# Kernel tuning notes

Hardware: AMD Instinct MI355X
Metric: run time of the kernel (lower is better)

The kernel has to match this reference:

```python
import jax, jax.numpy as jnp
import numpy as np

N = 50000        # number of nodes
K = 32           # sampled neighbors per node (fixed degree)
D = 128          # input_dim
DOUT = 128       # output_dim


def setup_inputs() -> dict:
    key = jax.random.key(0)
    k1, k2, k3, k4, k5 = jax.random.split(key, 5)
    node_fea1 = jax.random.normal(k1, (N, D), dtype=jnp.float32)
    node_fea2 = jax.random.normal(k2, (N, D), dtype=jnp.float32)
    neigh_idx1 = jax.random.randint(k3, (N, K), 0, N, dtype=jnp.int32)
    neigh_idx2 = jax.random.randint(k4, (N, K), 0, N, dtype=jnp.int32)
    # xavier-uniform init for weight [4*D, DOUT]
    limit = float(np.sqrt(6.0 / (4 * D + DOUT)))
    weight = jax.random.uniform(k5, (4 * D, DOUT), dtype=jnp.float32,
                                minval=-limit, maxval=limit)
    return {"node_fea1": node_fea1, "node_fea2": node_fea2,
            "neigh_idx1": neigh_idx1, "neigh_idx2": neigh_idx2,
            "weight": weight}


def reference(node_fea1, node_fea2, neigh_idx1, neigh_idx2, weight):
    # neighbor mean aggregation of node_fea1 over the two neighbor lists
    # (forward_den reads node_fea1 in BOTH aggregation blocks)
    nei1 = node_fea1[neigh_idx1].mean(axis=1)   # [N, D]
    nei2 = node_fea1[neigh_idx2].mean(axis=1)   # [N, D]
    cat_fea = jnp.concatenate([node_fea1, node_fea2, nei1, nei2], axis=1)  # [N, 4D]
    return jnp.tanh(cat_fea @ weight)           # [N, DOUT]
```

## Files before the change

### kernel.cpp

```cpp
#include <hip/hip_runtime.h>
#include <math.h>

#define N_NODES 50000
#define KNEI    32
#define DIM     128
#define DOUT    128
#define NUNITS  (2 * N_NODES)

typedef __attribute__((ext_vector_type(8))) short short8;
typedef __attribute__((ext_vector_type(4))) float floatx4;

static __device__ __forceinline__ unsigned short f2bf(float f) {
    unsigned int u = __float_as_uint(f);
    unsigned int lsb = (u >> 16) & 1u;
    u += 0x7fffu + lsb;
    return (unsigned short)(u >> 16);
}
static __device__ __forceinline__ unsigned int pack2(float a, float b) {
    return (unsigned int)f2bf(a) | ((unsigned int)f2bf(b) << 16);
}
static __device__ __forceinline__ float fast_tanh(float x) {
    float ax = fabsf(x);
    float e  = __expf(2.0f * ax);
    float t  = 1.0f - 2.0f / (e + 1.0f);
    return copysignf(t, x);
}
static __device__ __forceinline__ unsigned int pk4_u8(float a, float b, float c,
                                                      float d, float inv) {
    int qa = ((int)rintf(a * inv) + 128) & 0xff;
    int qb = ((int)rintf(b * inv) + 128) & 0xff;
    int qc = ((int)rintf(c * inv) + 128) & 0xff;
    int qd = ((int)rintf(d * inv) + 128) & 0xff;
    return (unsigned int)(qa | (qb << 8) | (qc << 16) | (qd << 24));
}


__global__ __launch_bounds__(256) void convert_i8(
    const float* __restrict__ src, unsigned int* __restrict__ Q8,
    float* __restrict__ Sc)
{
    int t = blockIdx.x * 256 + threadIdx.x;
    if (t >= N_NODES * 8) return;
    int node = t >> 3, j = t & 7;
    const float* rp = src + node * DIM + j * 16;
    float4 v0 = *(const float4*)rp;
    float4 v1 = *(const float4*)(rp + 4);
    float4 v2 = *(const float4*)(rp + 8);
    float4 v3 = *(const float4*)(rp + 12);

    float am = fabsf(v0.x);
    am = fmaxf(am, fabsf(v0.y)); am = fmaxf(am, fabsf(v0.z)); am = fmaxf(am, fabsf(v0.w));
    am = fmaxf(am, fabsf(v1.x)); am = fmaxf(am, fabsf(v1.y));
    am = fmaxf(am, fabsf(v1.z)); am = fmaxf(am, fabsf(v1.w));
    am = fmaxf(am, fabsf(v2.x)); am = fmaxf(am, fabsf(v2.y));
    am = fmaxf(am, fabsf(v2.z)); am = fmaxf(am, fabsf(v2.w));
    am = fmaxf(am, fabsf(v3.x)); am = fmaxf(am, fabsf(v3.y));
    am = fmaxf(am, fabsf(v3.z)); am = fmaxf(am, fabsf(v3.w));
    #pragma unroll
    for (int d = 1; d < 8; d <<= 1) am = fmaxf(am, __shfl_xor(am, d, 64));

    float inv = (am > 1e-30f) ? 127.0f / am : 0.0f;
    int4 o;
    o.x = (int)pk4_u8(v0.x, v0.y, v0.z, v0.w, inv);
    o.y = (int)pk4_u8(v1.x, v1.y, v1.z, v1.w, inv);
    o.z = (int)pk4_u8(v2.x, v2.y, v2.z, v2.w, inv);
    o.w = (int)pk4_u8(v3.x, v3.y, v3.z, v3.w, inv);
    *(int4*)(Q8 + node * 32 + j * 4) = o;
    if (j == 0) Sc[node] = am * (1.0f / 127.0f);
}

__global__ __launch_bounds__(256) void transpose_w(
    const float* __restrict__ W, unsigned short* __restrict__ Wt)
{
    int t = blockIdx.x * 256 + threadIdx.x;
    int k = t >> 7, n = t & 127;
    Wt[n * 512 + k] = f2bf(W[t]);
}

__global__ __launch_bounds__(256) void aggregate_i8(
    const unsigned char* __restrict__ Q8,
    const float* __restrict__ Sc,
    const int* __restrict__ idx1,
    const int* __restrict__ idx2,
    unsigned short* __restrict__ NEI)
{
    __shared__ int   idxs[32][40];
    __shared__ float scs[32][40];

    const int tid = threadIdx.x;
    const int bu0 = blockIdx.x * 32;
    const int ul  = tid >> 3;
    const int l   = tid & 7;

    {
        int uu = bu0 + ul;
        const int* ip = ((uu & 1) ? idx2 : idx1) + (uu >> 1) * KNEI + l * 4;
        int4 v = *(const int4*)ip;
        *(int4*)&idxs[ul][l * 4] = v;
    }
    __syncthreads();

    {
        #pragma unroll
        for (int k = 0; k < 4; ++k)
            scs[ul][l * 4 + k] = Sc[idxs[ul][l * 4 + k]];
    }
    __syncthreads();

    const int u    = bu0 + ul;
    const int node = u >> 1;
    const int list = u & 1;

    const unsigned char* base = Q8 + l * 16;
    float sums[16];
    #pragma unroll
    for (int i = 0; i < 16; ++i) sums[i] = 0.f;
    float ssum = 0.f;

    #pragma unroll 2
    for (int b = 0; b < 4; ++b) {
        int4 i4a = *(const int4*)&idxs[ul][b * 8];
        int4 i4b = *(const int4*)&idxs[ul][b * 8 + 4];
        int rows[8] = {i4a.x, i4a.y, i4a.z, i4a.w,
                       i4b.x, i4b.y, i4b.z, i4b.w};
        int4 v[8];
        #pragma unroll
        for (int j = 0; j < 8; ++j)
            v[j] = *(const int4*)(base + (size_t)rows[j] * 128);

        float4 sA = *(const float4*)&scs[ul][b * 8];
        float4 sB = *(const float4*)&scs[ul][b * 8 + 4];
        float sc8[8] = {sA.x, sA.y, sA.z, sA.w, sB.x, sB.y, sB.z, sB.w};
        ssum += sA.x + sA.y + sA.z + sA.w + sB.x + sB.y + sB.z + sB.w;

        #pragma unroll
        for (int j = 0; j < 8; ++j) {
            float s = sc8[j];
            unsigned int d[4] = {(unsigned int)v[j].x, (unsigned int)v[j].y,
                                 (unsigned int)v[j].z, (unsigned int)v[j].w};
            #pragma unroll
            for (int jj = 0; jj < 4; ++jj) {
                unsigned int w = d[jj];
                sums[4 * jj + 0] = fmaf(s, (float)(w & 0xffu),         sums[4 * jj + 0]);
                sums[4 * jj + 1] = fmaf(s, (float)((w >> 8) & 0xffu),  sums[4 * jj + 1]);
                sums[4 * jj + 2] = fmaf(s, (float)((w >> 16) & 0xffu), sums[4 * jj + 2]);
                sums[4 * jj + 3] = fmaf(s, (float)(w >> 24),           sums[4 * jj + 3]);
            }
        }
    }

    const float invK = 1.0f / 32.0f;
    const float corr = 128.0f * ssum;
    #pragma unroll
    for (int i = 0; i < 16; ++i) sums[i] = (sums[i] - corr) * invK;

    int4 o0, o1;
    o0.x = (int)pack2(sums[0],  sums[1]);
    o0.y = (int)pack2(sums[2],  sums[3]);
    o0.z = (int)pack2(sums[4],  sums[5]);
    o0.w = (int)pack2(sums[6],  sums[7]);
    o1.x = (int)pack2(sums[8],  sums[9]);
    o1.y = (int)pack2(sums[10], sums[11]);
    o1.z = (int)pack2(sums[12], sums[13]);
    o1.w = (int)pack2(sums[14], sums[15]);
    unsigned short* op = NEI + node * 256 + list * 128 + l * 16;
    *(int4*)op       = o0;
    *(int4*)(op + 8) = o1;
}

__global__ __launch_bounds__(256) void gemm128(
    const float*          __restrict__ fea1,
    const float*          __restrict__ fea2,
    const unsigned short* __restrict__ NEI,
    const unsigned short* __restrict__ Wt,
    float* __restrict__ out)
{
    __shared__ unsigned short As[128][72];
    __shared__ unsigned short Bs[128][72];

    const int tid  = threadIdx.x;
    const int w    = tid >> 6;
    const int lane = tid & 63;
    const int m0   = blockIdx.x * 128;
    const int wm   = (w & 1) * 64;
    const int wn   = (w >> 1) * 64;
    const int lm   = lane & 15;
    const int lk   = (lane >> 4) * 8;

    floatx4 acc[4][4];
    #pragma unroll
    for (int i = 0; i < 4; ++i)
        #pragma unroll
        for (int j = 0; j < 4; ++j)
            acc[i][j] = (floatx4){0.f, 0.f, 0.f, 0.f};

    for (int cc = 0; cc < 8; ++cc) {
        const int kb = cc * 64;
        if (cc < 4) {
            const float* src = (cc < 2) ? fea1 : fea2;
            const int cbase = (cc & 1) * 64;
            #pragma unroll
            for (int i = 0; i < 8; ++i) {
                int f   = tid + i * 256;
                int row = f >> 4;
                int c4  = (f & 15) * 4;
                int node = m0 + row;
                if (node >= N_NODES) node = N_NODES - 1;
                float4 v = *(const float4*)(src + node * DIM + cbase + c4);
                *(unsigned int*)&As[row][c4 + 0] = pack2(v.x, v.y);
                *(unsigned int*)&As[row][c4 + 2] = pack2(v.z, v.w);
            }
        } else {
            const int cb = kb - 256;
            #pragma unroll
            for (int i = 0; i < 4; ++i) {
                int sl  = tid + i * 256;
                int row = sl >> 3;
                int o8  = (sl & 7) * 8;
                int node = m0 + row;
                if (node >= N_NODES) node = N_NODES - 1;
                *(int4*)&As[row][o8] = *(const int4*)(NEI + node * 256 + cb + o8);
            }
        }
        #pragma unroll
        for (int i = 0; i < 4; ++i) {
            int sl  = tid + i * 256;
            int row = sl >> 3;
            int o8  = (sl & 7) * 8;
            *(int4*)&Bs[row][o8] = *(const int4*)(Wt + row * 512 + kb + o8);
        }
        __syncthreads();

        #pragma unroll
        for (int ks = 0; ks < 64; ks += 32) {
            short8 af[4], bf_[4];
            #pragma unroll
            for (int im = 0; im < 4; ++im)
                af[im] = *(const short8*)&As[wm + im * 16 + lm][ks + lk];
            #pragma unroll
            for (int in = 0; in < 4; ++in)
                bf_[in] = *(const short8*)&Bs[wn + in * 16 + lm][ks + lk];
            #pragma unroll
            for (int im = 0; im < 4; ++im)
                #pragma unroll
                for (int in = 0; in < 4; ++in)
                    acc[im][in] = __builtin_amdgcn_mfma_f32_16x16x32_bf16(
                        af[im], bf_[in], acc[im][in], 0, 0, 0);
        }
        __syncthreads();
    }

    #pragma unroll
    for (int im = 0; im < 4; ++im) {
        int rbase = m0 + wm + im * 16 + (lane >> 4) * 4;
        #pragma unroll
        for (int in = 0; in < 4; ++in) {
            int col = wn + in * 16 + lm;
            #pragma unroll
            for (int r = 0; r < 4; ++r) {
                int node = rbase + r;
                if (node < N_NODES)
                    out[node * DOUT + col] = fast_tanh(acc[im][in][r]);
            }
        }
    }
}

#define MT      64
#define KC      64
#define AS_STRIDE 68

__global__ __launch_bounds__(256) void sage_fused_fb(
    const float* __restrict__ fea1, const float* __restrict__ fea2,
    const int* __restrict__ idx1, const int* __restrict__ idx2,
    const float* __restrict__ W, float* __restrict__ out)
{
    __shared__ float As[KC][AS_STRIDE];
    __shared__ int   idxs[MT][64];
    const int tid = threadIdx.x;
    const int n0  = blockIdx.x * MT;
    #pragma unroll
    for (int i = 0; i < 8; ++i) {
        int e = tid + i * 256, m = e >> 5, kk = e & 31;
        int node = n0 + m; if (node >= N_NODES) node = N_NODES - 1;
        idxs[m][kk]      = idx1[node * KNEI + kk];
        idxs[m][32 + kk] = idx2[node * KNEI + kk];
    }
    float acc[8][4];
    #pragma unroll
    for (int i = 0; i < 8; ++i)
        #pragma unroll
        for (int j = 0; j < 4; ++j) acc[i][j] = 0.f;
    const int j0 = (tid & 31) * 4;
    const int m0 = (tid >> 5) * 8;
    for (int c = 0; c < 8; ++c) {
        if (c < 4) {
            const float* src = (c < 2) ? fea1 : fea2;
            const int cbase = (c & 1) * 64;
            #pragma unroll
            for (int i = 0; i < 4; ++i) {
                int f = tid + i * 256, m = f >> 4, c4 = (f & 15) * 4;
                int node = n0 + m; if (node >= N_NODES) node = N_NODES - 1;
                float4 v = *(const float4*)(src + node * DIM + cbase + c4);
                As[c4 + 0][m] = v.x; As[c4 + 1][m] = v.y;
                As[c4 + 2][m] = v.z; As[c4 + 3][m] = v.w;
            }
        } else {
            const int col = tid & 63, kbase = (c & 1) * 64;
            const int lbase = (c < 6) ? 0 : 32, g = tid >> 6;
            for (int mm = 0; mm < 16; ++mm) {
                const int m = g * 16 + mm;
                const int4* ip = (const int4*)&idxs[m][lbase];
                float s = 0.f;
                #pragma unroll
                for (int q = 0; q < 8; ++q) {
                    int4 nb = ip[q];
                    s += fea1[nb.x * DIM + kbase + col];
                    s += fea1[nb.y * DIM + kbase + col];
                    s += fea1[nb.z * DIM + kbase + col];
                    s += fea1[nb.w * DIM + kbase + col];
                }
                As[col][m] = s * (1.0f / 32.0f);
            }
        }
        __syncthreads();
        const float* wp = W + (c * KC) * DOUT + j0;
        #pragma unroll 4
        for (int k = 0; k < KC; ++k) {
            float4 w4 = *(const float4*)(wp + k * DOUT);
            const float4* ap = (const float4*)&As[k][m0];
            float4 a0 = ap[0]; float4 a1 = ap[1];
            float av[8] = {a0.x, a0.y, a0.z, a0.w, a1.x, a1.y, a1.z, a1.w};
            #pragma unroll
            for (int i = 0; i < 8; ++i) {
                acc[i][0] += av[i] * w4.x; acc[i][1] += av[i] * w4.y;
                acc[i][2] += av[i] * w4.z; acc[i][3] += av[i] * w4.w;
            }
        }
        __syncthreads();
    }
    #pragma unroll
    for (int i = 0; i < 8; ++i) {
        int node = n0 + m0 + i;
        if (node < N_NODES) {
            float4 r;
            r.x = tanhf(acc[i][0]); r.y = tanhf(acc[i][1]);
            r.z = tanhf(acc[i][2]); r.w = tanhf(acc[i][3]);
            *(float4*)(out + node * DOUT + j0) = r;
        }
    }
}

extern "C" void kernel_launch(void* const* d_in, const int* in_sizes, int n_in,
                              void* d_out, int out_size, void* d_ws, size_t ws_size,
                              hipStream_t stream) {
    const float* fea1 = (const float*)d_in[0];
    const float* fea2 = (const float*)d_in[1];
    const int*   idx1 = (const int*)d_in[2];
    const int*   idx2 = (const int*)d_in[3];
    const float* W    = (const float*)d_in[4];
    float* out = (float*)d_out;

    const size_t Q8_BYTES  = (size_t)N_NODES * DIM;
    const size_t SC_BYTES  = (size_t)N_NODES * 4;
    const size_t NEI_BYTES = (size_t)N_NODES * 256 * 2;
    const size_t WT_BYTES  = (size_t)512 * 128 * 2;

    if (ws_size >= Q8_BYTES + SC_BYTES + NEI_BYTES + WT_BYTES) {
        unsigned char*  Q8  = (unsigned char*)d_ws;
        float*          Scp = (float*)((char*)d_ws + Q8_BYTES);
        unsigned short* NEI = (unsigned short*)((char*)d_ws + Q8_BYTES + SC_BYTES);
        unsigned short* Wt  = (unsigned short*)((char*)d_ws + Q8_BYTES + SC_BYTES + NEI_BYTES);

        convert_i8<<<(N_NODES * 8 + 255) / 256, 256, 0, stream>>>(
            fea1, (unsigned int*)Q8, Scp);
        transpose_w<<<512 * 128 / 256, 256, 0, stream>>>(W, Wt);
        aggregate_i8<<<NUNITS / 32, 256, 0, stream>>>(Q8, Scp, idx1, idx2, NEI);
        gemm128<<<(N_NODES + 127) / 128, 256, 0, stream>>>(fea1, fea2, NEI, Wt, out);
    } else {
        const int grid = (N_NODES + MT - 1) / MT;
        sage_fused_fb<<<grid, 256, 0, stream>>>(fea1, fea2, idx1, idx2, W, out);
    }
}
```

Baseline: 165.4 us.

## Fuse neighbor aggregation into GEMM and merge conversion kernels

The int8 neighbor gather-mean now runs inside the GEMM's K-loop and writes straight into the shared A tile, so the bf16 NEI intermediate is never written to or read back from global memory. The GEMM M-tile shrinks from 128 to 64 rows to raise the block count. The feature quantization and weight transpose are merged into one launch, cutting the pipeline from four kernels to two. In exchange, each block's aggregation phase is serialized with its MFMA phase, with no separate high-occupancy gather kernel to hide gather latency, and the scale loads are now per-thread global reads.

```diff
diff --git a/kernel.cpp b/kernel.cpp
--- a/kernel.cpp
+++ b/kernel.cpp
@@ -5,7 +5,6 @@
 #define KNEI    32
 #define DIM     128
 #define DOUT    128
-#define NUNITS  (2 * N_NODES)
 
 typedef __attribute__((ext_vector_type(8))) short short8;
 typedef __attribute__((ext_vector_type(4))) float floatx4;
@@ -35,14 +34,22 @@
 }
 
 
-__global__ __launch_bounds__(256) void convert_i8(
-    const float* __restrict__ src, unsigned int* __restrict__ Q8,
-    float* __restrict__ Sc)
+__global__ __launch_bounds__(256) void convert_both(
+    const float* __restrict__ fea1, const float* __restrict__ W,
+    unsigned int* __restrict__ Q8, float* __restrict__ Sc,
+    unsigned short* __restrict__ Wt)
 {
-    int t = blockIdx.x * 256 + threadIdx.x;
+    int b = blockIdx.x;
+    if (b >= 1563) {
+        int t = (b - 1563) * 256 + threadIdx.x;
+        int k = t >> 7, n = t & 127;
+        Wt[n * 512 + k] = f2bf(W[t]);
+        return;
+    }
+    int t = b * 256 + threadIdx.x;
     if (t >= N_NODES * 8) return;
     int node = t >> 3, j = t & 7;
-    const float* rp = src + node * DIM + j * 16;
+    const float* rp = fea1 + node * DIM + j * 16;
     float4 v0 = *(const float4*)rp;
     float4 v1 = *(const float4*)(rp + 4);
     float4 v2 = *(const float4*)(rp + 8);
@@ -69,138 +76,49 @@
     if (j == 0) Sc[node] = am * (1.0f / 127.0f);
 }
 
-__global__ __launch_bounds__(256) void transpose_w(
-    const float* __restrict__ W, unsigned short* __restrict__ Wt)
-{
-    int t = blockIdx.x * 256 + threadIdx.x;
-    int k = t >> 7, n = t & 127;
-    Wt[n * 512 + k] = f2bf(W[t]);
-}
-
-__global__ __launch_bounds__(256) void aggregate_i8(
-    const unsigned char* __restrict__ Q8,
-    const float* __restrict__ Sc,
-    const int* __restrict__ idx1,
-    const int* __restrict__ idx2,
-    unsigned short* __restrict__ NEI)
-{
-    __shared__ int   idxs[32][40];
-    __shared__ float scs[32][40];
-
-    const int tid = threadIdx.x;
-    const int bu0 = blockIdx.x * 32;
-    const int ul  = tid >> 3;
-    const int l   = tid & 7;
-
-    {
-        int uu = bu0 + ul;
-        const int* ip = ((uu & 1) ? idx2 : idx1) + (uu >> 1) * KNEI + l * 4;
-        int4 v = *(const int4*)ip;
-        *(int4*)&idxs[ul][l * 4] = v;
-    }
-    __syncthreads();
-
-    {
-        #pragma unroll
-        for (int k = 0; k < 4; ++k)
-            scs[ul][l * 4 + k] = Sc[idxs[ul][l * 4 + k]];
-    }
-    __syncthreads();
-
-    const int u    = bu0 + ul;
-    const int node = u >> 1;
-    const int list = u & 1;
-
-    const unsigned char* base = Q8 + l * 16;
-    float sums[16];
-    #pragma unroll
-    for (int i = 0; i < 16; ++i) sums[i] = 0.f;
-    float ssum = 0.f;
-
-    #pragma unroll 2
-    for (int b = 0; b < 4; ++b) {
-        int4 i4a = *(const int4*)&idxs[ul][b * 8];
-        int4 i4b = *(const int4*)&idxs[ul][b * 8 + 4];
-        int rows[8] = {i4a.x, i4a.y, i4a.z, i4a.w,
-                       i4b.x, i4b.y, i4b.z, i4b.w};
-        int4 v[8];
-        #pragma unroll
-        for (int j = 0; j < 8; ++j)
-            v[j] = *(const int4*)(base + (size_t)rows[j] * 128);
-
-        float4 sA = *(const float4*)&scs[ul][b * 8];
-        float4 sB = *(const float4*)&scs[ul][b * 8 + 4];
-        float sc8[8] = {sA.x, sA.y, sA.z, sA.w, sB.x, sB.y, sB.z, sB.w};
-        ssum += sA.x + sA.y + sA.z + sA.w + sB.x + sB.y + sB.z + sB.w;
-
-        #pragma unroll
-        for (int j = 0; j < 8; ++j) {
-            float s = sc8[j];
-            unsigned int d[4] = {(unsigned int)v[j].x, (unsigned int)v[j].y,
-                                 (unsigned int)v[j].z, (unsigned int)v[j].w};
-            #pragma unroll
-            for (int jj = 0; jj < 4; ++jj) {
-                unsigned int w = d[jj];
-                sums[4 * jj + 0] = fmaf(s, (float)(w & 0xffu),         sums[4 * jj + 0]);
-                sums[4 * jj + 1] = fmaf(s, (float)((w >> 8) & 0xffu),  sums[4 * jj + 1]);
-                sums[4 * jj + 2] = fmaf(s, (float)((w >> 16) & 0xffu), sums[4 * jj + 2]);
-                sums[4 * jj + 3] = fmaf(s, (float)(w >> 24),           sums[4 * jj + 3]);
-            }
-        }
-    }
-
-    const float invK = 1.0f / 32.0f;
-    const float corr = 128.0f * ssum;
-    #pragma unroll
-    for (int i = 0; i < 16; ++i) sums[i] = (sums[i] - corr) * invK;
-
-    int4 o0, o1;
-    o0.x = (int)pack2(sums[0],  sums[1]);
-    o0.y = (int)pack2(sums[2],  sums[3]);
-    o0.z = (int)pack2(sums[4],  sums[5]);
-    o0.w = (int)pack2(sums[6],  sums[7]);
-    o1.x = (int)pack2(sums[8],  sums[9]);
-    o1.y = (int)pack2(sums[10], sums[11]);
-    o1.z = (int)pack2(sums[12], sums[13]);
-    o1.w = (int)pack2(sums[14], sums[15]);
-    unsigned short* op = NEI + node * 256 + list * 128 + l * 16;
-    *(int4*)op       = o0;
-    *(int4*)(op + 8) = o1;
-}
-
-__global__ __launch_bounds__(256) void gemm128(
+__global__ __launch_bounds__(256) void gemm_fused(
     const float*          __restrict__ fea1,
     const float*          __restrict__ fea2,
-    const unsigned short* __restrict__ NEI,
+    const unsigned char*  __restrict__ Q8,
+    const float*          __restrict__ Sc,
+    const int*            __restrict__ idx1,
+    const int*            __restrict__ idx2,
     const unsigned short* __restrict__ Wt,
     float* __restrict__ out)
 {
-    __shared__ unsigned short As[128][72];
+    __shared__ unsigned short As[64][72];
     __shared__ unsigned short Bs[128][72];
 
     const int tid  = threadIdx.x;
     const int w    = tid >> 6;
     const int lane = tid & 63;
-    const int m0   = blockIdx.x * 128;
-    const int wm   = (w & 1) * 64;
+    const int m0   = blockIdx.x * 64;
+    const int wm   = (w & 1) * 32;
     const int wn   = (w >> 1) * 64;
     const int lm   = lane & 15;
     const int lk   = (lane >> 4) * 8;
 
-    floatx4 acc[4][4];
-    #pragma unroll
-    for (int i = 0; i < 4; ++i)
+    floatx4 acc[2][4];
+    #pragma unroll
+    for (int i = 0; i < 2; ++i)
         #pragma unroll
         for (int j = 0; j < 4; ++j)
             acc[i][j] = (floatx4){0.f, 0.f, 0.f, 0.f};
 
     for (int cc = 0; cc < 8; ++cc) {
         const int kb = cc * 64;
+        #pragma unroll
+        for (int i = 0; i < 4; ++i) {
+            int sl  = tid + i * 256;
+            int row = sl >> 3;
+            int o8  = (sl & 7) * 8;
+            *(int4*)&Bs[row][o8] = *(const int4*)(Wt + row * 512 + kb + o8);
+        }
         if (cc < 4) {
             const float* src = (cc < 2) ? fea1 : fea2;
             const int cbase = (cc & 1) * 64;
             #pragma unroll
-            for (int i = 0; i < 8; ++i) {
+            for (int i = 0; i < 4; ++i) {
                 int f   = tid + i * 256;
                 int row = f >> 4;
                 int c4  = (f & 15) * 4;
@@ -211,37 +129,82 @@
                 *(unsigned int*)&As[row][c4 + 2] = pack2(v.z, v.w);
             }
         } else {
-            const int cb = kb - 256;
-            #pragma unroll
-            for (int i = 0; i < 4; ++i) {
-                int sl  = tid + i * 256;
-                int row = sl >> 3;
-                int o8  = (sl & 7) * 8;
-                int node = m0 + row;
-                if (node >= N_NODES) node = N_NODES - 1;
-                *(int4*)&As[row][o8] = *(const int4*)(NEI + node * 256 + cb + o8);
-            }
-        }
-        #pragma unroll
-        for (int i = 0; i < 4; ++i) {
-            int sl  = tid + i * 256;
-            int row = sl >> 3;
-            int o8  = (sl & 7) * 8;
-            *(int4*)&Bs[row][o8] = *(const int4*)(Wt + row * 512 + kb + o8);
+            const int* ibase = (cc >= 6) ? idx2 : idx1;
+            const int cb = (cc & 1) * 64;
+            const int g  = tid >> 2;
+            const int l2 = tid & 3;
+            int node = m0 + g;
+            if (node >= N_NODES) node = N_NODES - 1;
+            const int4* ip = (const int4*)(ibase + node * KNEI);
+            int4 I[8];
+            #pragma unroll
+            for (int q = 0; q < 8; ++q) I[q] = ip[q];
+
+            const unsigned char* qb = Q8 + cb + l2 * 16;
+            float sums[16];
+            #pragma unroll
+            for (int i = 0; i < 16; ++i) sums[i] = 0.f;
+            float ssum = 0.f;
+
+            #pragma unroll 2
+            for (int q = 0; q < 8; ++q) {
+                int r4[4] = {I[q].x, I[q].y, I[q].z, I[q].w};
+                #pragma unroll
+                for (int t4 = 0; t4 < 4; ++t4) {
+                    unsigned int row = (unsigned int)r4[t4];
+                    uint4 v = *(const uint4*)(qb + row * 128u);
+                    float s = Sc[row];
+                    ssum += s;
+                    unsigned int d0 = v.x, d1 = v.y, d2 = v.z, d3 = v.w;
+                    sums[0]  = fmaf(s, (float)(d0 & 0xffu),         sums[0]);
+                    sums[1]  = fmaf(s, (float)((d0 >> 8) & 0xffu),  sums[1]);
+                    sums[2]  = fmaf(s, (float)((d0 >> 16) & 0xffu), sums[2]);
+                    sums[3]  = fmaf(s, (float)(d0 >> 24),           sums[3]);
+                    sums[4]  = fmaf(s, (float)(d1 & 0xffu),         sums[4]);
+                    sums[5]  = fmaf(s, (float)((d1 >> 8) & 0xffu),  sums[5]);
+                    sums[6]  = fmaf(s, (float)((d1 >> 16) & 0xffu), sums[6]);
+                    sums[7]  = fmaf(s, (float)(d1 >> 24),           sums[7]);
+                    sums[8]  = fmaf(s, (float)(d2 & 0xffu),         sums[8]);
+                    sums[9]  = fmaf(s, (float)((d2 >> 8) & 0xffu),  sums[9]);
+                    sums[10] = fmaf(s, (float)((d2 >> 16) & 0xffu), sums[10]);
+                    sums[11] = fmaf(s, (float)(d2 >> 24),           sums[11]);
+                    sums[12] = fmaf(s, (float)(d3 & 0xffu),         sums[12]);
+                    sums[13] = fmaf(s, (float)((d3 >> 8) & 0xffu),  sums[13]);
+                    sums[14] = fmaf(s, (float)((d3 >> 16) & 0xffu), sums[14]);
+                    sums[15] = fmaf(s, (float)(d3 >> 24),           sums[15]);
+                }
+            }
+            const float inv32 = 1.0f / 32.0f;
+            const float corr  = 128.0f * ssum;
+            #pragma unroll
+            for (int i = 0; i < 16; ++i) sums[i] = (sums[i] - corr) * inv32;
+
+            unsigned short* ap = &As[g][l2 * 16];
+            int4 oA, oB;
+            oA.x = (int)pack2(sums[0],  sums[1]);
+            oA.y = (int)pack2(sums[2],  sums[3]);
+            oA.z = (int)pack2(sums[4],  sums[5]);
+            oA.w = (int)pack2(sums[6],  sums[7]);
+            oB.x = (int)pack2(sums[8],  sums[9]);
+            oB.y = (int)pack2(sums[10], sums[11]);
+            oB.z = (int)pack2(sums[12], sums[13]);
+            oB.w = (int)pack2(sums[14], sums[15]);
+            *(int4*)ap       = oA;
+            *(int4*)(ap + 8) = oB;
         }
         __syncthreads();
 
         #pragma unroll
         for (int ks = 0; ks < 64; ks += 32) {
-            short8 af[4], bf_[4];
-            #pragma unroll
-            for (int im = 0; im < 4; ++im)
+            short8 af[2], bf_[4];
+            #pragma unroll
+            for (int im = 0; im < 2; ++im)
                 af[im] = *(const short8*)&As[wm + im * 16 + lm][ks + lk];
             #pragma unroll
             for (int in = 0; in < 4; ++in)
                 bf_[in] = *(const short8*)&Bs[wn + in * 16 + lm][ks + lk];
             #pragma unroll
-            for (int im = 0; im < 4; ++im)
+            for (int im = 0; im < 2; ++im)
                 #pragma unroll
                 for (int in = 0; in < 4; ++in)
                     acc[im][in] = __builtin_amdgcn_mfma_f32_16x16x32_bf16(
@@ -251,7 +214,7 @@
     }
 
     #pragma unroll
-    for (int im = 0; im < 4; ++im) {
+    for (int im = 0; im < 2; ++im) {
         int rbase = m0 + wm + im * 16 + (lane >> 4) * 4;
         #pragma unroll
         for (int in = 0; in < 4; ++in) {
@@ -363,20 +326,17 @@
 
     const size_t Q8_BYTES  = (size_t)N_NODES * DIM;
     const size_t SC_BYTES  = (size_t)N_NODES * 4;
-    const size_t NEI_BYTES = (size_t)N_NODES * 256 * 2;
     const size_t WT_BYTES  = (size_t)512 * 128 * 2;
 
-    if (ws_size >= Q8_BYTES + SC_BYTES + NEI_BYTES + WT_BYTES) {
+    if (ws_size >= Q8_BYTES + SC_BYTES + WT_BYTES) {
         unsigned char*  Q8  = (unsigned char*)d_ws;
         float*          Scp = (float*)((char*)d_ws + Q8_BYTES);
-        unsigned short* NEI = (unsigned short*)((char*)d_ws + Q8_BYTES + SC_BYTES);
-        unsigned short* Wt  = (unsigned short*)((char*)d_ws + Q8_BYTES + SC_BYTES + NEI_BYTES);
-
-        convert_i8<<<(N_NODES * 8 + 255) / 256, 256, 0, stream>>>(
-            fea1, (unsigned int*)Q8, Scp);
-        transpose_w<<<512 * 128 / 256, 256, 0, stream>>>(W, Wt);
-        aggregate_i8<<<NUNITS / 32, 256, 0, stream>>>(Q8, Scp, idx1, idx2, NEI);
-        gemm128<<<(N_NODES + 127) / 128, 256, 0, stream>>>(fea1, fea2, NEI, Wt, out);
+        unsigned short* Wt  = (unsigned short*)((char*)d_ws + Q8_BYTES + SC_BYTES);
+
+        convert_both<<<1563 + 256, 256, 0, stream>>>(
+            fea1, W, (unsigned int*)Q8, Scp, Wt);
+        gemm_fused<<<(N_NODES + 63) / 64, 256, 0, stream>>>(
+            fea1, fea2, Q8, Scp, idx1, idx2, Wt, out);
     } else {
         const int grid = (N_NODES + MT - 1) / MT;
         sage_fused_fb<<<grid, 256, 0, stream>>>(fea1, fea2, idx1, idx2, W, out);
```

Result: slower. 239.2 us (+44.6%).

## Split int8 feature table into two column planes and aggregate per plane

Applied to the files above, without the earlier changes.

The quantized int8 feature table is stored as two 64-byte column planes, and the neighbor aggregation runs as two launches, each gathering one plane. Each launch's gather working set is then 3.2 MB instead of 6.4 MB, which is meant to improve cache hit rates for the random row gathers. The quantize kernel and the weight transpose are merged into one launch, and the index loads and output stores now use nontemporal hints. The cost is an extra launch, a second read of the index lists and scales, and 64-byte gathers that may use memory transactions less efficiently.

```diff
diff --git a/kernel.cpp b/kernel.cpp
--- a/kernel.cpp
+++ b/kernel.cpp
@@ -9,6 +9,7 @@
 
 typedef __attribute__((ext_vector_type(8))) short short8;
 typedef __attribute__((ext_vector_type(4))) float floatx4;
+typedef __attribute__((ext_vector_type(4))) int  intx4;
 
 static __device__ __forceinline__ unsigned short f2bf(float f) {
     unsigned int u = __float_as_uint(f);
@@ -35,14 +36,22 @@
 }
 
 
-__global__ __launch_bounds__(256) void convert_i8(
-    const float* __restrict__ src, unsigned int* __restrict__ Q8,
-    float* __restrict__ Sc)
+__global__ __launch_bounds__(256) void convert_both(
+    const float* __restrict__ fea1, const float* __restrict__ W,
+    unsigned char* __restrict__ Q8, float* __restrict__ Sc,
+    unsigned short* __restrict__ Wt)
 {
-    int t = blockIdx.x * 256 + threadIdx.x;
+    int b = blockIdx.x;
+    if (b >= 1563) {
+        int t = (b - 1563) * 256 + threadIdx.x;
+        int k = t >> 7, n = t & 127;
+        Wt[n * 512 + k] = f2bf(W[t]);
+        return;
+    }
+    int t = b * 256 + threadIdx.x;
     if (t >= N_NODES * 8) return;
     int node = t >> 3, j = t & 7;
-    const float* rp = src + node * DIM + j * 16;
+    const float* rp = fea1 + node * DIM + j * 16;
     float4 v0 = *(const float4*)rp;
     float4 v1 = *(const float4*)(rp + 4);
     float4 v2 = *(const float4*)(rp + 8);
@@ -60,58 +69,63 @@
     for (int d = 1; d < 8; d <<= 1) am = fmaxf(am, __shfl_xor(am, d, 64));
 
     float inv = (am > 1e-30f) ? 127.0f / am : 0.0f;
-    int4 o;
-    o.x = (int)pk4_u8(v0.x, v0.y, v0.z, v0.w, inv);
-    o.y = (int)pk4_u8(v1.x, v1.y, v1.z, v1.w, inv);
-    o.z = (int)pk4_u8(v2.x, v2.y, v2.z, v2.w, inv);
-    o.w = (int)pk4_u8(v3.x, v3.y, v3.z, v3.w, inv);
-    *(int4*)(Q8 + node * 32 + j * 4) = o;
+    uint4 o;
+    o.x = pk4_u8(v0.x, v0.y, v0.z, v0.w, inv);
+    o.y = pk4_u8(v1.x, v1.y, v1.z, v1.w, inv);
+    o.z = pk4_u8(v2.x, v2.y, v2.z, v2.w, inv);
+    o.w = pk4_u8(v3.x, v3.y, v3.z, v3.w, inv);
+    unsigned char* qp = Q8 + (size_t)(j >> 2) * (N_NODES * 64)
+                           + (size_t)node * 64 + (j & 3) * 16;
+    *(uint4*)qp = o;
     if (j == 0) Sc[node] = am * (1.0f / 127.0f);
 }
 
-__global__ __launch_bounds__(256) void transpose_w(
-    const float* __restrict__ W, unsigned short* __restrict__ Wt)
-{
-    int t = blockIdx.x * 256 + threadIdx.x;
-    int k = t >> 7, n = t & 127;
-    Wt[n * 512 + k] = f2bf(W[t]);
-}
-
-__global__ __launch_bounds__(256) void aggregate_i8(
+__global__ __launch_bounds__(256) void aggregate_plane(
     const unsigned char* __restrict__ Q8,
     const float* __restrict__ Sc,
     const int* __restrict__ idx1,
     const int* __restrict__ idx2,
-    unsigned short* __restrict__ NEI)
+    unsigned short* __restrict__ NEI,
+    const int plane)
 {
-    __shared__ int   idxs[32][40];
-    __shared__ float scs[32][40];
+    __shared__ int   idxs[64][36];
+    __shared__ float scs[64][36];
 
     const int tid = threadIdx.x;
-    const int bu0 = blockIdx.x * 32;
-    const int ul  = tid >> 3;
-    const int l   = tid & 7;
-
-    {
-        int uu = bu0 + ul;
-        const int* ip = ((uu & 1) ? idx2 : idx1) + (uu >> 1) * KNEI + l * 4;
-        int4 v = *(const int4*)ip;
-        *(int4*)&idxs[ul][l * 4] = v;
+    const int bu0 = blockIdx.x * 64;
+    const int ul  = tid >> 2;
+    const int l   = tid & 3;
+
+    #pragma unroll
+    for (int i = 0; i < 2; ++i) {
+        int s   = tid + i * 256;
+        int us  = s >> 3;
+        int off = (s & 7) * 4;
+        int uu  = bu0 + us;
+        if (uu >= NUNITS) uu = NUNITS - 1;
+        const int* ip = ((uu & 1) ? idx2 : idx1) + (uu >> 1) * KNEI + off;
+        intx4 v = __builtin_nontemporal_load((const intx4*)ip);
+        *(intx4*)&idxs[us][off] = v;
     }
     __syncthreads();
 
-    {
+    #pragma unroll
+    for (int i = 0; i < 2; ++i) {
+        int s   = tid + i * 256;
+        int us  = s >> 3;
+        int off = (s & 7) * 4;
         #pragma unroll
         for (int k = 0; k < 4; ++k)
-            scs[ul][l * 4 + k] = Sc[idxs[ul][l * 4 + k]];
+            scs[us][off + k] = Sc[idxs[us][off + k]];
     }
     __syncthreads();
 
     const int u    = bu0 + ul;
-    const int node = u >> 1;
-    const int list = u & 1;
-
-    const unsigned char* base = Q8 + l * 16;
+    const int cu   = (u < NUNITS) ? u : (NUNITS - 1);
+    const int node = cu >> 1;
+    const int list = cu & 1;
+
+    const unsigned char* qb = Q8 + (size_t)plane * (N_NODES * 64) + l * 16;
     float sums[16];
     #pragma unroll
     for (int i = 0; i < 16; ++i) sums[i] = 0.f;
@@ -123,10 +137,10 @@
         int4 i4b = *(const int4*)&idxs[ul][b * 8 + 4];
         int rows[8] = {i4a.x, i4a.y, i4a.z, i4a.w,
                        i4b.x, i4b.y, i4b.z, i4b.w};
-        int4 v[8];
+        uint4 v[8];
         #pragma unroll
         for (int j = 0; j < 8; ++j)
-            v[j] = *(const int4*)(base + (size_t)rows[j] * 128);
+            v[j] = *(const uint4*)(qb + (size_t)rows[j] * 64);
 
         float4 sA = *(const float4*)&scs[ul][b * 8];
         float4 sB = *(const float4*)&scs[ul][b * 8 + 4];
@@ -136,16 +150,23 @@
         #pragma unroll
         for (int j = 0; j < 8; ++j) {
             float s = sc8[j];
-            unsigned int d[4] = {(unsigned int)v[j].x, (unsigned int)v[j].y,
-                                 (unsigned int)v[j].z, (unsigned int)v[j].w};
-            #pragma unroll
-            for (int jj = 0; jj < 4; ++jj) {
-                unsigned int w = d[jj];
-                sums[4 * jj + 0] = fmaf(s, (float)(w & 0xffu),         sums[4 * jj + 0]);
-                sums[4 * jj + 1] = fmaf(s, (float)((w >> 8) & 0xffu),  sums[4 * jj + 1]);
-                sums[4 * jj + 2] = fmaf(s, (float)((w >> 16) & 0xffu), sums[4 * jj + 2]);
-                sums[4 * jj + 3] = fmaf(s, (float)(w >> 24),           sums[4 * jj + 3]);
-            }
+            unsigned int d0 = v[j].x, d1 = v[j].y, d2 = v[j].z, d3 = v[j].w;
+            sums[0]  = fmaf(s, (float)(d0 & 0xffu),         sums[0]);
+            sums[1]  = fmaf(s, (float)((d0 >> 8) & 0xffu),  sums[1]);
+            sums[2]  = fmaf(s, (float)((d0 >> 16) & 0xffu), sums[2]);
+            sums[3]  = fmaf(s, (float)(d0 >> 24),           sums[3]);
+            sums[4]  = fmaf(s, (float)(d1 & 0xffu),         sums[4]);
+            sums[5]  = fmaf(s, (float)((d1 >> 8) & 0xffu),  sums[5]);
+            sums[6]  = fmaf(s, (float)((d1 >> 16) & 0xffu), sums[6]);
+            sums[7]  = fmaf(s, (float)(d1 >> 24),           sums[7]);
+            sums[8]  = fmaf(s, (float)(d2 & 0xffu),         sums[8]);
+            sums[9]  = fmaf(s, (float)((d2 >> 8) & 0xffu),  sums[9]);
+            sums[10] = fmaf(s, (float)((d2 >> 16) & 0xffu), sums[10]);
+            sums[11] = fmaf(s, (float)(d2 >> 24),           sums[11]);
+            sums[12] = fmaf(s, (float)(d3 & 0xffu),         sums[12]);
+            sums[13] = fmaf(s, (float)((d3 >> 8) & 0xffu),  sums[13]);
+            sums[14] = fmaf(s, (float)((d3 >> 16) & 0xffu), sums[14]);
+            sums[15] = fmaf(s, (float)(d3 >> 24),           sums[15]);
         }
     }
 
@@ -154,18 +175,20 @@
     #pragma unroll
     for (int i = 0; i < 16; ++i) sums[i] = (sums[i] - corr) * invK;
 
-    int4 o0, o1;
-    o0.x = (int)pack2(sums[0],  sums[1]);
-    o0.y = (int)pack2(sums[2],  sums[3]);
-    o0.z = (int)pack2(sums[4],  sums[5]);
-    o0.w = (int)pack2(sums[6],  sums[7]);
-    o1.x = (int)pack2(sums[8],  sums[9]);
-    o1.y = (int)pack2(sums[10], sums[11]);
-    o1.z = (int)pack2(sums[12], sums[13]);
-    o1.w = (int)pack2(sums[14], sums[15]);
-    unsigned short* op = NEI + node * 256 + list * 128 + l * 16;
-    *(int4*)op       = o0;
-    *(int4*)(op + 8) = o1;
+    if (u < NUNITS) {
+        intx4 o0, o1;
+        o0.x = (int)pack2(sums[0],  sums[1]);
+        o0.y = (int)pack2(sums[2],  sums[3]);
+        o0.z = (int)pack2(sums[4],  sums[5]);
+        o0.w = (int)pack2(sums[6],  sums[7]);
+        o1.x = (int)pack2(sums[8],  sums[9]);
+        o1.y = (int)pack2(sums[10], sums[11]);
+        o1.z = (int)pack2(sums[12], sums[13]);
+        o1.w = (int)pack2(sums[14], sums[15]);
+        unsigned short* op = NEI + node * 256 + list * 128 + plane * 64 + l * 16;
+        __builtin_nontemporal_store(o0, (intx4*)op);
+        __builtin_nontemporal_store(o1, (intx4*)(op + 8));
+    }
 }
 
 __global__ __launch_bounds__(256) void gemm128(
@@ -372,10 +395,10 @@
         unsigned short* NEI = (unsigned short*)((char*)d_ws + Q8_BYTES + SC_BYTES);
         unsigned short* Wt  = (unsigned short*)((char*)d_ws + Q8_BYTES + SC_BYTES + NEI_BYTES);
 
-        convert_i8<<<(N_NODES * 8 + 255) / 256, 256, 0, stream>>>(
-            fea1, (unsigned int*)Q8, Scp);
-        transpose_w<<<512 * 128 / 256, 256, 0, stream>>>(W, Wt);
-        aggregate_i8<<<NUNITS / 32, 256, 0, stream>>>(Q8, Scp, idx1, idx2, NEI);
+        convert_both<<<1563 + 256, 256, 0, stream>>>(fea1, W, Q8, Scp, Wt);
+        const int agrid = (NUNITS + 63) / 64;
+        aggregate_plane<<<agrid, 256, 0, stream>>>(Q8, Scp, idx1, idx2, NEI, 0);
+        aggregate_plane<<<agrid, 256, 0, stream>>>(Q8, Scp, idx1, idx2, NEI, 1);
         gemm128<<<(N_NODES + 127) / 128, 256, 0, stream>>>(fea1, fea2, NEI, Wt, out);
     } else {
         const int grid = (N_NODES + MT - 1) / MT;
```

Result: slower. 193.0 us (+16.7%).

## Split GEMM and co-schedule self-feature half with neighbor aggregation

Applied to the files above, without the earlier changes.

Merges the int8 conversion and weight transpose into one launch. Splits the GEMM so the fea1/fea2 half of K runs in the same launch as the gather aggregation, writing fp32 partial sums to a workspace. A second GEMM handles the neighbor half and adds the partials before tanh. The aim is to overlap compute-bound MFMA blocks with the memory-latency-bound gather and to cut launch count. In exchange it writes and reads back a 25.6 MB fp32 partial buffer, and the larger shared-memory footprint may lower aggregation occupancy.

```diff
diff --git a/kernel.cpp b/kernel.cpp
--- a/kernel.cpp
+++ b/kernel.cpp
@@ -6,6 +6,9 @@
 #define DIM     128
 #define DOUT    128
 #define NUNITS  (2 * N_NODES)
+
+#define GP1_BLOCKS 391
+#define AGG_BLOCKS (NUNITS / 32)
 
 typedef __attribute__((ext_vector_type(8))) short short8;
 typedef __attribute__((ext_vector_type(4))) float floatx4;
@@ -35,14 +38,22 @@
 }
 
 
-__global__ __launch_bounds__(256) void convert_i8(
-    const float* __restrict__ src, unsigned int* __restrict__ Q8,
-    float* __restrict__ Sc)
+__global__ __launch_bounds__(256) void convert_both(
+    const float* __restrict__ fea1, const float* __restrict__ W,
+    unsigned int* __restrict__ Q8, float* __restrict__ Sc,
+    unsigned short* __restrict__ Wt)
 {
-    int t = blockIdx.x * 256 + threadIdx.x;
+    int b = blockIdx.x;
+    if (b >= 1563) {
+        int t = (b - 1563) * 256 + threadIdx.x;
+        int k = t >> 7, n = t & 127;
+        Wt[n * 512 + k] = f2bf(W[t]);
+        return;
+    }
+    int t = b * 256 + threadIdx.x;
     if (t >= N_NODES * 8) return;
     int node = t >> 3, j = t & 7;
-    const float* rp = src + node * DIM + j * 16;
+    const float* rp = fea1 + node * DIM + j * 16;
     float4 v0 = *(const float4*)rp;
     float4 v1 = *(const float4*)(rp + 4);
     float4 v2 = *(const float4*)(rp + 8);
@@ -69,26 +80,103 @@
     if (j == 0) Sc[node] = am * (1.0f / 127.0f);
 }
 
-__global__ __launch_bounds__(256) void transpose_w(
-    const float* __restrict__ W, unsigned short* __restrict__ Wt)
+__global__ __launch_bounds__(256) void agg_or_gemmp1(
+    const float*          __restrict__ fea1,
+    const float*          __restrict__ fea2,
+    const unsigned char*  __restrict__ Q8,
+    const float*          __restrict__ Sc,
+    const int*            __restrict__ idx1,
+    const int*            __restrict__ idx2,
+    const unsigned short* __restrict__ Wt,
+    unsigned short*       __restrict__ NEI,
+    float*                __restrict__ part)
 {
-    int t = blockIdx.x * 256 + threadIdx.x;
-    int k = t >> 7, n = t & 127;
-    Wt[n * 512 + k] = f2bf(W[t]);
-}
-
-__global__ __launch_bounds__(256) void aggregate_i8(
-    const unsigned char* __restrict__ Q8,
-    const float* __restrict__ Sc,
-    const int* __restrict__ idx1,
-    const int* __restrict__ idx2,
-    unsigned short* __restrict__ NEI)
-{
-    __shared__ int   idxs[32][40];
-    __shared__ float scs[32][40];
-
+    __shared__ unsigned char smem[36864];
     const int tid = threadIdx.x;
-    const int bu0 = blockIdx.x * 32;
+
+    if (blockIdx.x < GP1_BLOCKS) {
+        unsigned short (*As)[72] = (unsigned short(*)[72])smem;
+        unsigned short (*Bs)[72] = (unsigned short(*)[72])(smem + 18432);
+
+        const int w    = tid >> 6;
+        const int lane = tid & 63;
+        const int m0   = blockIdx.x * 128;
+        const int wm   = (w & 1) * 64;
+        const int wn   = (w >> 1) * 64;
+        const int lm   = lane & 15;
+        const int lk   = (lane >> 4) * 8;
+
+        floatx4 acc[4][4];
+        #pragma unroll
+        for (int i = 0; i < 4; ++i)
+            #pragma unroll
+            for (int j = 0; j < 4; ++j)
+                acc[i][j] = (floatx4){0.f, 0.f, 0.f, 0.f};
+
+        for (int cc = 0; cc < 4; ++cc) {
+            const int kb = cc * 64;
+            const float* src = (cc < 2) ? fea1 : fea2;
+            const int cbase = (cc & 1) * 64;
+            #pragma unroll
+            for (int i = 0; i < 8; ++i) {
+                int f   = tid + i * 256;
+                int row = f >> 4;
+                int c4  = (f & 15) * 4;
+                int node = m0 + row;
+                if (node >= N_NODES) node = N_NODES - 1;
+                float4 v = *(const float4*)(src + node * DIM + cbase + c4);
+                *(unsigned int*)&As[row][c4 + 0] = pack2(v.x, v.y);
+                *(unsigned int*)&As[row][c4 + 2] = pack2(v.z, v.w);
+            }
+            #pragma unroll
+            for (int i = 0; i < 4; ++i) {
+                int sl  = tid + i * 256;
+                int row = sl >> 3;
+                int o8  = (sl & 7) * 8;
+                *(int4*)&Bs[row][o8] = *(const int4*)(Wt + row * 512 + kb + o8);
+            }
+            __syncthreads();
+
+            #pragma unroll
+            for (int ks = 0; ks < 64; ks += 32) {
+                short8 af[4], bf_[4];
+                #pragma unroll
+                for (int im = 0; im < 4; ++im)
+                    af[im] = *(const short8*)&As[wm + im * 16 + lm][ks + lk];
+                #pragma unroll
+                for (int in = 0; in < 4; ++in)
+                    bf_[in] = *(const short8*)&Bs[wn + in * 16 + lm][ks + lk];
+                #pragma unroll
+                for (int im = 0; im < 4; ++im)
+                    #pragma unroll
+                    for (int in = 0; in < 4; ++in)
+                        acc[im][in] = __builtin_amdgcn_mfma_f32_16x16x32_bf16(
+                            af[im], bf_[in], acc[im][in], 0, 0, 0);
+            }
+            __syncthreads();
+        }
+
+        #pragma unroll
+        for (int im = 0; im < 4; ++im) {
+            int rbase = m0 + wm + im * 16 + (lane >> 4) * 4;
+            #pragma unroll
+            for (int in = 0; in < 4; ++in) {
+                int col = wn + in * 16 + lm;
+                #pragma unroll
+                for (int r = 0; r < 4; ++r) {
+                    int node = rbase + r;
+                    if (node < N_NODES)
+                        part[node * DOUT + col] = acc[im][in][r];
+                }
+            }
+        }
+        return;
+    }
+
+    int (*idxs)[40]  = (int(*)[40])smem;
+    float (*scs)[40] = (float(*)[40])(smem + 5120);
+
+    const int bu0 = (blockIdx.x - GP1_BLOCKS) * 32;
     const int ul  = tid >> 3;
     const int l   = tid & 7;
 
@@ -99,7 +187,6 @@
         *(int4*)&idxs[ul][l * 4] = v;
     }
     __syncthreads();
-
     {
         #pragma unroll
         for (int k = 0; k < 4; ++k)
@@ -123,10 +210,10 @@
         int4 i4b = *(const int4*)&idxs[ul][b * 8 + 4];
         int rows[8] = {i4a.x, i4a.y, i4a.z, i4a.w,
                        i4b.x, i4b.y, i4b.z, i4b.w};
-        int4 v[8];
+        uint4 v[8];
         #pragma unroll
         for (int j = 0; j < 8; ++j)
-            v[j] = *(const int4*)(base + (size_t)rows[j] * 128);
+            v[j] = *(const uint4*)(base + (size_t)rows[j] * 128);
 
         float4 sA = *(const float4*)&scs[ul][b * 8];
         float4 sB = *(const float4*)&scs[ul][b * 8 + 4];
@@ -136,16 +223,23 @@
         #pragma unroll
         for (int j = 0; j < 8; ++j) {
             float s = sc8[j];
-            unsigned int d[4] = {(unsigned int)v[j].x, (unsigned int)v[j].y,
-                                 (unsigned int)v[j].z, (unsigned int)v[j].w};
-            #pragma unroll
-            for (int jj = 0; jj < 4; ++jj) {
-                unsigned int w = d[jj];
-                sums[4 * jj + 0] = fmaf(s, (float)(w & 0xffu),         sums[4 * jj + 0]);
-                sums[4 * jj + 1] = fmaf(s, (float)((w >> 8) & 0xffu),  sums[4 * jj + 1]);
-                sums[4 * jj + 2] = fmaf(s, (float)((w >> 16) & 0xffu), sums[4 * jj + 2]);
-                sums[4 * jj + 3] = fmaf(s, (float)(w >> 24),           sums[4 * jj + 3]);
-            }
+            unsigned int d0 = v[j].x, d1 = v[j].y, d2 = v[j].z, d3 = v[j].w;
+            sums[0]  = fmaf(s, (float)(d0 & 0xffu),         sums[0]);
+            sums[1]  = fmaf(s, (float)((d0 >> 8) & 0xffu),  sums[1]);
+            sums[2]  = fmaf(s, (float)((d0 >> 16) & 0xffu), sums[2]);
+            sums[3]  = fmaf(s, (float)(d0 >> 24),           sums[3]);
+            sums[4]  = fmaf(s, (float)(d1 & 0xffu),         sums[4]);
+            sums[5]  = fmaf(s, (float)((d1 >> 8) & 0xffu),  sums[5]);
+            sums[6]  = fmaf(s, (float)((d1 >> 16) & 0xffu), sums[6]);
+            sums[7]  = fmaf(s, (float)(d1 >> 24),           sums[7]);
+            sums[8]  = fmaf(s, (float)(d2 & 0xffu),         sums[8]);
+            sums[9]  = fmaf(s, (float)((d2 >> 8) & 0xffu),  sums[9]);
+            sums[10] = fmaf(s, (float)((d2 >> 16) & 0xffu), sums[10]);
+            sums[11] = fmaf(s, (float)(d2 >> 24),           sums[11]);
+            sums[12] = fmaf(s, (float)(d3 & 0xffu),         sums[12]);
+            sums[13] = fmaf(s, (float)((d3 >> 8) & 0xffu),  sums[13]);
+            sums[14] = fmaf(s, (float)((d3 >> 16) & 0xffu), sums[14]);
+            sums[15] = fmaf(s, (float)(d3 >> 24),           sums[15]);
         }
     }
 
@@ -168,11 +262,10 @@
     *(int4*)(op + 8) = o1;
 }
 
-__global__ __launch_bounds__(256) void gemm128(
-    const float*          __restrict__ fea1,
-    const float*          __restrict__ fea2,
+__global__ __launch_bounds__(256) void gemm_p2(
     const unsigned short* __restrict__ NEI,
     const unsigned short* __restrict__ Wt,
+    const float*          __restrict__ part,
     float* __restrict__ out)
 {
     __shared__ unsigned short As[128][72];
@@ -194,33 +287,17 @@
         for (int j = 0; j < 4; ++j)
             acc[i][j] = (floatx4){0.f, 0.f, 0.f, 0.f};
 
-    for (int cc = 0; cc < 8; ++cc) {
-        const int kb = cc * 64;
-        if (cc < 4) {
-            const float* src = (cc < 2) ? fea1 : fea2;
-            const int cbase = (cc & 1) * 64;
-            #pragma unroll
-            for (int i = 0; i < 8; ++i) {
-                int f   = tid + i * 256;
-                int row = f >> 4;
-                int c4  = (f & 15) * 4;
-                int node = m0 + row;
-                if (node >= N_NODES) node = N_NODES - 1;
-                float4 v = *(const float4*)(src + node * DIM + cbase + c4);
-                *(unsigned int*)&As[row][c4 + 0] = pack2(v.x, v.y);
-                *(unsigned int*)&As[row][c4 + 2] = pack2(v.z, v.w);
-            }
-        } else {
-            const int cb = kb - 256;
-            #pragma unroll
-            for (int i = 0; i < 4; ++i) {
-                int sl  = tid + i * 256;
-                int row = sl >> 3;
-                int o8  = (sl & 7) * 8;
-                int node = m0 + row;
-                if (node >= N_NODES) node = N_NODES - 1;
-                *(int4*)&As[row][o8] = *(const int4*)(NEI + node * 256 + cb + o8);
-            }
+    for (int cc = 0; cc < 4; ++cc) {
+        const int kb = 256 + cc * 64;
+        const int cb = cc * 64;
+        #pragma unroll
+        for (int i = 0; i < 4; ++i) {
+            int sl  = tid + i * 256;
+            int row = sl >> 3;
+            int o8  = (sl & 7) * 8;
+            int node = m0 + row;
+            if (node >= N_NODES) node = N_NODES - 1;
+            *(int4*)&As[row][o8] = *(const int4*)(NEI + node * 256 + cb + o8);
         }
         #pragma unroll
         for (int i = 0; i < 4; ++i) {
@@ -260,7 +337,8 @@
             for (int r = 0; r < 4; ++r) {
                 int node = rbase + r;
                 if (node < N_NODES)
-                    out[node * DOUT + col] = fast_tanh(acc[im][in][r]);
+                    out[node * DOUT + col] =
+                        fast_tanh(acc[im][in][r] + part[node * DOUT + col]);
             }
         }
     }
@@ -361,22 +439,24 @@
     const float* W    = (const float*)d_in[4];
     float* out = (float*)d_out;
 
-    const size_t Q8_BYTES  = (size_t)N_NODES * DIM;
-    const size_t SC_BYTES  = (size_t)N_NODES * 4;
-    const size_t NEI_BYTES = (size_t)N_NODES * 256 * 2;
-    const size_t WT_BYTES  = (size_t)512 * 128 * 2;
-
-    if (ws_size >= Q8_BYTES + SC_BYTES + NEI_BYTES + WT_BYTES) {
+    const size_t Q8_BYTES   = (size_t)N_NODES * DIM;
+    const size_t SC_BYTES   = (size_t)N_NODES * 4;
+    const size_t NEI_BYTES  = (size_t)N_NODES * 256 * 2;
+    const size_t WT_BYTES   = (size_t)512 * 128 * 2;
+    const size_t PART_BYTES = (size_t)N_NODES * DOUT * 4;
+
+    if (ws_size >= Q8_BYTES + SC_BYTES + NEI_BYTES + WT_BYTES + PART_BYTES) {
         unsigned char*  Q8  = (unsigned char*)d_ws;
         float*          Scp = (float*)((char*)d_ws + Q8_BYTES);
         unsigned short* NEI = (unsigned short*)((char*)d_ws + Q8_BYTES + SC_BYTES);
         unsigned short* Wt  = (unsigned short*)((char*)d_ws + Q8_BYTES + SC_BYTES + NEI_BYTES);
-
-        convert_i8<<<(N_NODES * 8 + 255) / 256, 256, 0, stream>>>(
-            fea1, (unsigned int*)Q8, Scp);
-        transpose_w<<<512 * 128 / 256, 256, 0, stream>>>(W, Wt);
-        aggregate_i8<<<NUNITS / 32, 256, 0, stream>>>(Q8, Scp, idx1, idx2, NEI);
-        gemm128<<<(N_NODES + 127) / 128, 256, 0, stream>>>(fea1, fea2, NEI, Wt, out);
+        float*          Pp  = (float*)((char*)d_ws + Q8_BYTES + SC_BYTES + NEI_BYTES + WT_BYTES);
+
+        convert_both<<<1563 + 256, 256, 0, stream>>>(
+            fea1, W, (unsigned int*)Q8, Scp, Wt);
+        agg_or_gemmp1<<<GP1_BLOCKS + AGG_BLOCKS, 256, 0, stream>>>(
+            fea1, fea2, Q8, Scp, idx1, idx2, Wt, NEI, Pp);
+        gemm_p2<<<GP1_BLOCKS, 256, 0, stream>>>(NEI, Wt, Pp, out);
     } else {
         const int grid = (N_NODES + MT - 1) / MT;
         sage_fused_fb<<<grid, 256, 0, stream>>>(fea1, fea2, idx1, idx2, W, out);
```

New measurement: 189.8 us. +14.8%, slower.
